# Kernel tuning notes

Measured on AMD Instinct MI355X. Metric: run time of the kernel, lower is better.

## Reference

```python
import jax, jax.numpy as jnp
import numpy as np

WS, SHIFT, NH, DIM = 8, 4, 4, 128
HD = DIM // NH
B, H, W = 16, 128, 128
N = WS * WS
LOG100 = float(np.log(100.0))


def _rel_tables():
    r = np.arange(-(WS - 1), WS, dtype=np.float32)
    tab = np.stack(np.meshgrid(r, r, indexing='ij'), axis=-1) / (WS - 1) * 8.0
    tab = np.sign(tab) * np.log2(np.abs(tab) + 1.0) / np.log2(8.0)
    coords = np.stack(np.meshgrid(np.arange(WS), np.arange(WS), indexing='ij')).reshape(2, -1)
    rel = (coords[:, :, None] - coords[:, None, :]).transpose(1, 2, 0).copy()
    rel[:, :, 0] += WS - 1
    rel[:, :, 1] += WS - 1
    rel[:, :, 0] *= 2 * WS - 1
    return jnp.asarray(tab.reshape(-1, 2)), jnp.asarray(rel.sum(-1))

REL_TABLE, REL_INDEX = _rel_tables()  # ((2WS-1)^2, 2), (N, N)


def _attn_mask():
    img = np.zeros((H, W), np.float32)
    cnt = 0
    for hs in (slice(0, -WS), slice(-WS, -SHIFT), slice(-SHIFT, None)):
        for ws in (slice(0, -WS), slice(-WS, -SHIFT), slice(-SHIFT, None)):
            img[hs, ws] = cnt
            cnt += 1
    mw = img.reshape(H // WS, WS, W // WS, WS).transpose(0, 2, 1, 3).reshape(-1, N)
    d = mw[:, None, :] - mw[:, :, None]
    return jnp.asarray(np.where(d != 0, -100.0, 0.0).astype(np.float32))

ATTN_MASK = _attn_mask()  # (nW, N, N)


def _ln(x, w, b, eps=1e-5):
    mu = x.mean(-1, keepdims=True)
    var = ((x - mu) ** 2).mean(-1, keepdims=True)
    return (x - mu) * jax.lax.rsqrt(var + eps) * w + b


def setup_inputs() -> dict:
    key = jax.random.key(0)
    ks = jax.random.split(key, 8)
    s = 0.02
    return {
        'x': jax.random.normal(ks[0], (B, DIM, H, W), jnp.float32),
        'norm1_w': jnp.ones((DIM,), jnp.float32),
        'norm1_b': jnp.zeros((DIM,), jnp.float32),
        'qkv_w': jax.random.normal(ks[1], (3 * DIM, DIM), jnp.float32) * s,
        'q_bias': jnp.zeros((DIM,), jnp.float32),
        'v_bias': jnp.zeros((DIM,), jnp.float32),
        'logit_scale': jnp.full((NH, 1, 1), float(np.log(10.0)), jnp.float32),
        'cpb_w1': jax.random.normal(ks[2], (512, 2), jnp.float32) * s,
        'cpb_b1': jnp.zeros((512,), jnp.float32),
        'cpb_w2': jax.random.normal(ks[3], (NH, 512), jnp.float32) * s,
        'proj_w': jax.random.normal(ks[4], (DIM, DIM), jnp.float32) * s,
        'proj_b': jnp.zeros((DIM,), jnp.float32),
        'norm2_w': jnp.ones((DIM,), jnp.float32),
        'norm2_b': jnp.zeros((DIM,), jnp.float32),
        'fc1_w': jax.random.normal(ks[5], (4 * DIM, DIM), jnp.float32) * s,
        'fc1_b': jnp.zeros((4 * DIM,), jnp.float32),
        'fc2_w': jax.random.normal(ks[6], (DIM, 4 * DIM), jnp.float32) * s,
        'fc2_b': jnp.zeros((DIM,), jnp.float32),
    }


def reference(x, norm1_w, norm1_b, qkv_w, q_bias, v_bias, logit_scale,
              cpb_w1, cpb_b1, cpb_w2, proj_w, proj_b,
              norm2_w, norm2_b, fc1_w, fc1_b, fc2_w, fc2_b):
    xb = jnp.transpose(x, (0, 2, 3, 1))                 # (B,H,W,C)
    shortcut = xb.reshape(B, H * W, DIM)
    shifted = jnp.roll(xb, (-SHIFT, -SHIFT), axis=(1, 2))
    # window partition -> (B*nW, N, C)
    xw = shifted.reshape(B, H // WS, WS, W // WS, WS, DIM)
    xw = xw.transpose(0, 1, 3, 2, 4, 5).reshape(-1, N, DIM)
    B_ = xw.shape[0]
    qkv_bias = jnp.concatenate([q_bias, jnp.zeros_like(v_bias), v_bias])
    qkv = xw @ qkv_w.T + qkv_bias
    qkv = qkv.reshape(B_, N, 3, NH, HD).transpose(2, 0, 3, 1, 4)
    q, k, v = qkv[0], qkv[1], qkv[2]                    # (B_,NH,N,HD)
    qn = q / jnp.maximum(jnp.linalg.norm(q, axis=-1, keepdims=True), 1e-12)
    kn = k / jnp.maximum(jnp.linalg.norm(k, axis=-1, keepdims=True), 1e-12)
    attn = jnp.einsum('bhnd,bhmd->bhnm', qn, kn)
    attn = attn * jnp.exp(jnp.minimum(logit_scale, LOG100))
    # continuous relative position bias: tiny MLP over log-spaced coords + gather
    tab = jax.nn.relu(REL_TABLE @ cpb_w1.T + cpb_b1) @ cpb_w2.T    # ((2WS-1)^2, NH)
    bias = tab[REL_INDEX.reshape(-1)].reshape(N, N, NH).transpose(2, 0, 1)
    attn = attn + (16.0 * jax.nn.sigmoid(bias))[None]
    nW = ATTN_MASK.shape[0]
    attn = attn.reshape(B_ // nW, nW, NH, N, N) + ATTN_MASK[None, :, None]
    attn = jax.nn.softmax(attn.reshape(B_, NH, N, N), axis=-1)
    out = jnp.einsum('bhnm,bhmd->bhnd', attn, v).transpose(0, 2, 1, 3).reshape(B_, N, DIM)
    out = out @ proj_w.T + proj_b
    # window reverse + reverse cyclic shift
    out = out.reshape(B, H // WS, W // WS, WS, WS, DIM).transpose(0, 1, 3, 2, 4, 5).reshape(B, H, W, DIM)
    out = jnp.roll(out, (SHIFT, SHIFT), axis=(1, 2)).reshape(B, H * W, DIM)
    x1 = shortcut + _ln(out, norm1_w, norm1_b)          # Swin-v2 post-norm residual
    hdn = jax.nn.silu(x1 @ fc1_w.T + fc1_b) @ fc2_w.T + fc2_b
    x2 = x1 + _ln(hdn, norm2_w, norm2_b)
    return x2.reshape(B, H, W, DIM).transpose(0, 3, 1, 2)
```

## Files before the change

kernel.cpp:

```cpp
#include <hip/hip_runtime.h>
#include <cstdint>
#include <cstddef>

typedef __bf16 bf16;
typedef __bf16 bf16x8 __attribute__((ext_vector_type(8)));
typedef float f32x4 __attribute__((ext_vector_type(4)));

#define MFMA16(a, b, c) __builtin_amdgcn_mfma_f32_16x16x32_bf16((a), (b), (c), 0, 0, 0)

__device__ __forceinline__ float bf2f(bf16 v) { return (float)v; }

#define OFF_SCALES 65536
#define OFF_FLAG   65552
#define OFF_QKVB   65600
#define OFF_PROJB  67136
#define OFF_N1W    67648
#define OFF_N1B    68160
#define OFF_FC1B   68672
#define OFF_FC2B   70720
#define OFF_N2W    71232
#define OFF_N2B    71744
#define OFF_QKVW   73728
#define OFF_PROJW  172032
#define OFF_FC1W   204800
#define OFF_FC2W   335872

template<int DT>
__device__ __forceinline__ void g_ld4(const void* base, size_t idx, float* o) {
    if constexpr (DT == 0) {
        uint2 d = *(const uint2*)((const bf16*)base + idx);
        const bf16* p = (const bf16*)&d;
        o[0] = bf2f(p[0]); o[1] = bf2f(p[1]); o[2] = bf2f(p[2]); o[3] = bf2f(p[3]);
    } else {
        float4 d = *(const float4*)((const float*)base + idx);
        o[0] = d.x; o[1] = d.y; o[2] = d.z; o[3] = d.w;
    }
}

__global__ void k_precompute(const void* __restrict__ cpb_w1, const void* __restrict__ cpb_b1,
                             const void* __restrict__ cpb_w2, const void* __restrict__ logit_scale,
                             const void* __restrict__ qkv_w_raw,
                             float* __restrict__ biasAll, float* __restrict__ scales,
                             int* __restrict__ flag)
{
    __shared__ float w1s[1024];
    __shared__ float b1s[512];
    __shared__ float w2s[2048];
    __shared__ float tabv[225][4];
    __shared__ int s_cnt;
    const int t = threadIdx.x;
    if (t == 0) s_cnt = 0;
    __syncthreads();
    {
        const unsigned short* u = (const unsigned short*)qkv_w_raw;
        int c = 0;
        for (int i = t; i < 1024; i += 256) {
            const int e = (u[i] >> 7) & 0xFF;
            if (e >= 0x90 || (e != 0 && e <= 0x60)) ++c;
        }
        atomicAdd(&s_cnt, c);
    }
    __syncthreads();
    const int isf = (s_cnt > 64) ? 1 : 0;
    if (t == 0) *flag = isf;
    if (isf) {
        const float* w1 = (const float*)cpb_w1;
        const float* b1 = (const float*)cpb_b1;
        const float* w2 = (const float*)cpb_w2;
        for (int i = t; i < 1024; i += 256) w1s[i] = w1[i];
        for (int i = t; i < 512;  i += 256) b1s[i] = b1[i];
        for (int i = t; i < 2048; i += 256) w2s[i] = w2[i];
        if (t < 4) scales[t] = expf(fminf(((const float*)logit_scale)[t], 4.6051701859880914f));
    } else {
        const bf16* w1 = (const bf16*)cpb_w1;
        const bf16* b1 = (const bf16*)cpb_b1;
        const bf16* w2 = (const bf16*)cpb_w2;
        for (int i = t; i < 1024; i += 256) w1s[i] = bf2f(w1[i]);
        for (int i = t; i < 512;  i += 256) b1s[i] = bf2f(b1[i]);
        for (int i = t; i < 2048; i += 256) w2s[i] = bf2f(w2[i]);
        if (t < 4) scales[t] = expf(fminf(bf2f(((const bf16*)logit_scale)[t]), 4.6051701859880914f));
    }
    __syncthreads();
    if (t < 225) {
        const int i = t / 15, j = t % 15;
        auto relf = [](int tt) -> float {
            float tf = (float)tt * (8.0f / 7.0f);
            float a = log2f(fabsf(tf) + 1.0f) * (1.0f / 3.0f);
            return tt < 0 ? -a : a;
        };
        const float x0 = relf(i - 7), x1 = relf(j - 7);
        float a0 = 0.f, a1 = 0.f, a2 = 0.f, a3 = 0.f;
        for (int jj = 0; jj < 512; ++jj) {
            float hv = w1s[jj*2] * x0 + w1s[jj*2+1] * x1 + b1s[jj];
            hv = fmaxf(hv, 0.0f);
            a0 += w2s[jj]        * hv;
            a1 += w2s[512 + jj]  * hv;
            a2 += w2s[1024 + jj] * hv;
            a3 += w2s[1536 + jj] * hv;
        }
        tabv[t][0] = a0; tabv[t][1] = a1; tabv[t][2] = a2; tabv[t][3] = a3;
    }
    __syncthreads();
    for (int idx = t; idx < 4*64*64; idx += 256) {
        const int h = idx >> 12, rem = idx & 4095, i = rem >> 6, j = rem & 63;
        const int di = (i >> 3) - (j >> 3) + 7;
        const int dj = (i & 7) - (j & 7) + 7;
        const float bv = tabv[di*15 + dj][h];
        biasAll[idx] = 16.0f / (1.0f + expf(-bv));
    }
}

__global__ void k_convert(
    const void* __restrict__ qkv_w, const void* __restrict__ proj_w,
    const void* __restrict__ fc1w, const void* __restrict__ fc2w,
    const void* __restrict__ q_bias, const void* __restrict__ v_bias,
    const void* __restrict__ proj_b, const void* __restrict__ n1w, const void* __restrict__ n1b,
    const void* __restrict__ fc1b, const void* __restrict__ fc2b,
    const void* __restrict__ n2w, const void* __restrict__ n2b,
    const int* __restrict__ flag, char* __restrict__ ws)
{
    const int isf = *flag;
    const int g  = blockIdx.x * 256 + threadIdx.x;
    const int gs = gridDim.x * 256;
    bf16* qw = (bf16*)(ws + OFF_QKVW);
    bf16* pw = (bf16*)(ws + OFF_PROJW);
    bf16* f1 = (bf16*)(ws + OFF_FC1W);
    bf16* f2 = (bf16*)(ws + OFF_FC2W);
    if (isf) {
        const float* a = (const float*)qkv_w;  for (int i = g; i < 49152; i += gs) qw[i] = (bf16)a[i];
        const float* b = (const float*)proj_w; for (int i = g; i < 16384; i += gs) pw[i] = (bf16)b[i];
        const float* c = (const float*)fc1w;   for (int i = g; i < 65536; i += gs) f1[i] = (bf16)c[i];
        const float* d = (const float*)fc2w;   for (int i = g; i < 65536; i += gs) f2[i] = (bf16)d[i];
    } else {
        const bf16* a = (const bf16*)qkv_w;  for (int i = g; i < 49152; i += gs) qw[i] = a[i];
        const bf16* b = (const bf16*)proj_w; for (int i = g; i < 16384; i += gs) pw[i] = b[i];
        const bf16* c = (const bf16*)fc1w;   for (int i = g; i < 65536; i += gs) f1[i] = c[i];
        const bf16* d = (const bf16*)fc2w;   for (int i = g; i < 65536; i += gs) f2[i] = d[i];
    }
    auto ldf = [&](const void* p, int i) -> float {
        return isf ? ((const float*)p)[i] : bf2f(((const bf16*)p)[i]);
    };
    float* qb  = (float*)(ws + OFF_QKVB);
    float* pb  = (float*)(ws + OFF_PROJB);
    float* w1  = (float*)(ws + OFF_N1W);
    float* b1  = (float*)(ws + OFF_N1B);
    float* f1b = (float*)(ws + OFF_FC1B);
    float* f2b = (float*)(ws + OFF_FC2B);
    float* w2  = (float*)(ws + OFF_N2W);
    float* b2  = (float*)(ws + OFF_N2B);
    for (int i = g; i < 384; i += gs)
        qb[i] = (i < 128) ? ldf(q_bias, i) : ((i < 256) ? 0.0f : ldf(v_bias, i - 256));
    for (int i = g; i < 512; i += gs) f1b[i] = ldf(fc1b, i);
    for (int i = g; i < 128; i += gs) {
        pb[i]  = ldf(proj_b, i); w1[i] = ldf(n1w, i); b1[i] = ldf(n1b, i);
        f2b[i] = ldf(fc2b, i);   w2[i] = ldf(n2w, i); b2[i] = ldf(n2b, i);
    }
}

template<int DT>
__global__ __launch_bounds__(256, 2) void k_fused(
    const void* __restrict__ x,
    const bf16* __restrict__ qkvw, const float* __restrict__ qkvb,
    const bf16* __restrict__ projw, const float* __restrict__ projb,
    const float* __restrict__ n1wf, const float* __restrict__ n1bf,
    const bf16* __restrict__ fc1w, const float* __restrict__ fc1bf,
    const bf16* __restrict__ fc2w, const float* __restrict__ fc2bf,
    const float* __restrict__ n2wf, const float* __restrict__ n2bf,
    const float* __restrict__ biasAll, const float* __restrict__ scales,
    const int* __restrict__ flag, void* __restrict__ out)
{
    if (*flag != DT) return;

    __shared__ __align__(16) char smem[75008];
    bf16* Xs    = (bf16*)smem;
    bf16* qkvs  = (bf16*)(smem + 17408);
    bf16* Ps    = qkvs;
    bf16* x1s   = qkvs;
    bf16* vs    = (bf16*)(smem + 54272);
    bf16* Os    = vs;
    bf16* hs    = vs;
    float* invqs = (float*)(smem + 72704);
    float* invks = (float*)(smem + 73728);
    int*   rid   = (int*)(smem + 74752);
    float* psum = invqs;
    float* pvar = invks;

    const int tid  = threadIdx.x;
    const int wv   = tid >> 6;
    const int lane = tid & 63;
    const int l15  = lane & 15;
    const int quad = lane >> 4;

    const int bid0 = blockIdx.x;
    const int bid  = ((bid0 & 7) << 9) | (bid0 >> 3);
    const int b   = bid >> 8;
    const int wh  = (bid >> 4) & 15;
    const int ww  = bid & 15;

    {
        const int c  = tid & 127;
        const int rb = tid >> 7;
        const int w0 = ww*8 + 4;
        const int w1 = (ww*8 + 8) & 127;
#pragma unroll
        for (int k = 0; k < 4; ++k) {
            const int r    = k*2 + rb;
            const int srch = (wh*8 + r + 4) & 127;
            const size_t rowbase = (((size_t)(b*128 + c))*128 + srch)*128;
            float va[4], vb[4];
            g_ld4<DT>(x, rowbase + w0, va);
            g_ld4<DT>(x, rowbase + w1, vb);
#pragma unroll
            for (int j = 0; j < 4; ++j) {
                Xs[(r*8 + j)*136 + c]     = (bf16)va[j];
                Xs[(r*8 + 4 + j)*136 + c] = (bf16)vb[j];
            }
        }
        if (tid < 64) {
            const int rr = tid >> 3, cc = tid & 7;
            const int hs_ = wh*8 + rr, wsc = ww*8 + cc;
            const int rh = (hs_ < 120) ? 0 : ((hs_ < 124) ? 1 : 2);
            const int rw = (wsc < 120) ? 0 : ((wsc < 124) ? 1 : 2);
            rid[tid] = rh*3 + rw;
        }
    }
    __syncthreads();

    {
        f32x4 acc[4][6];
#pragma unroll
        for (int mt = 0; mt < 4; ++mt)
#pragma unroll
            for (int nl = 0; nl < 6; ++nl) acc[mt][nl] = (f32x4){0.f, 0.f, 0.f, 0.f};
#pragma unroll
        for (int ks = 0; ks < 4; ++ks) {
            bf16x8 a[4];
#pragma unroll
            for (int mt = 0; mt < 4; ++mt)
                a[mt] = *(const bf16x8*)&Xs[(mt*16 + l15)*136 + ks*32 + quad*8];
#pragma unroll
            for (int nl = 0; nl < 6; ++nl) {
                const int o = (wv*6 + nl)*16 + l15;
                bf16x8 bw = *(const bf16x8*)&qkvw[(size_t)o*128 + ks*32 + quad*8];
#pragma unroll
                for (int mt = 0; mt < 4; ++mt)
                    acc[mt][nl] = MFMA16(a[mt], bw, acc[mt][nl]);
            }
        }
#pragma unroll
        for (int nl = 0; nl < 6; ++nl) {
            const int col = (wv*6 + nl)*16 + l15;
            const float bias = qkvb[col];
#pragma unroll
            for (int mt = 0; mt < 4; ++mt)
#pragma unroll
                for (int r = 0; r < 4; ++r) {
                    const int row = mt*16 + quad*4 + r;
                    const float v = acc[mt][nl][r] + bias;
                    if (col < 256) qkvs[row*264 + col] = (bf16)v;
                    else           vs[(col - 256)*72 + row] = (bf16)v;
                }
        }
    }
    __syncthreads();

    {
        const int n = lane;
        const bf16* qrow = &qkvs[n*264 + wv*32];
        const bf16* krow = &qkvs[n*264 + 128 + wv*32];
        float sq = 0.f, sk = 0.f;
#pragma unroll
        for (int dd = 0; dd < 4; ++dd) {
            bf16x8 vq = *(const bf16x8*)(qrow + dd*8);
            bf16x8 vk = *(const bf16x8*)(krow + dd*8);
#pragma unroll
            for (int e = 0; e < 8; ++e) {
                const float fq = (float)vq[e]; sq += fq*fq;
                const float fk = (float)vk[e]; sk += fk*fk;
            }
        }
        invqs[wv*64 + n] = 1.0f / fmaxf(sqrtf(sq), 1e-12f);
        invks[wv*64 + n] = 1.0f / fmaxf(sqrtf(sk), 1e-12f);
    }
    __syncthreads();

    {
        const float scale = scales[wv];
        f32x4 s[4][4];
#pragma unroll
        for (int mt = 0; mt < 4; ++mt)
#pragma unroll
            for (int nt = 0; nt < 4; ++nt) s[mt][nt] = (f32x4){0.f, 0.f, 0.f, 0.f};
        bf16x8 aq[4];
#pragma unroll
        for (int mt = 0; mt < 4; ++mt)
            aq[mt] = *(const bf16x8*)&qkvs[(mt*16 + l15)*264 + wv*32 + quad*8];
#pragma unroll
        for (int nt = 0; nt < 4; ++nt) {
            bf16x8 bk = *(const bf16x8*)&qkvs[(nt*16 + l15)*264 + 128 + wv*32 + quad*8];
#pragma unroll
            for (int mt = 0; mt < 4; ++mt)
                s[mt][nt] = MFMA16(aq[mt], bk, s[mt][nt]);
        }
        __syncthreads();
        const float* bg = biasAll + wv*4096;
        const bool bnd = (wh == 15) || (ww == 15);
        float ikj[4]; int rj[4];
#pragma unroll
        for (int nt = 0; nt < 4; ++nt) {
            ikj[nt] = invks[wv*64 + nt*16 + l15];
            rj[nt]  = rid[nt*16 + l15];
        }
#pragma unroll
        for (int mt = 0; mt < 4; ++mt)
#pragma unroll
            for (int r = 0; r < 4; ++r) {
                const int i = mt*16 + quad*4 + r;
                const float iqs = invqs[wv*64 + i] * scale;
                const int ri = rid[i];
#pragma unroll
                for (int nt = 0; nt < 4; ++nt) {
                    const int j = nt*16 + l15;
                    float v = s[mt][nt][r] * (iqs * ikj[nt]) + bg[i*64 + j];
                    if (bnd && (ri != rj[nt])) v -= 100.0f;
                    s[mt][nt][r] = v;
                }
            }
#pragma unroll
        for (int mt = 0; mt < 4; ++mt) {
            float mx[4], sm[4];
#pragma unroll
            for (int r = 0; r < 4; ++r) {
                float m = fmaxf(fmaxf(s[mt][0][r], s[mt][1][r]), fmaxf(s[mt][2][r], s[mt][3][r]));
                m = fmaxf(m, __shfl_xor(m, 1));
                m = fmaxf(m, __shfl_xor(m, 2));
                m = fmaxf(m, __shfl_xor(m, 4));
                m = fmaxf(m, __shfl_xor(m, 8));
                mx[r] = m; sm[r] = 0.f;
            }
#pragma unroll
            for (int nt = 0; nt < 4; ++nt)
#pragma unroll
                for (int r = 0; r < 4; ++r) {
                    const float e = __expf(s[mt][nt][r] - mx[r]);
                    s[mt][nt][r] = e;
                    sm[r] += e;
                }
#pragma unroll
            for (int r = 0; r < 4; ++r) {
                float t2 = sm[r];
                t2 += __shfl_xor(t2, 1);
                t2 += __shfl_xor(t2, 2);
                t2 += __shfl_xor(t2, 4);
                t2 += __shfl_xor(t2, 8);
                sm[r] = 1.0f / t2;
            }
#pragma unroll
            for (int nt = 0; nt < 4; ++nt)
#pragma unroll
                for (int r = 0; r < 4; ++r) {
                    const float p = s[mt][nt][r] * sm[r];
                    Ps[wv*64*72 + (mt*16 + quad*4 + r)*72 + nt*16 + l15] = (bf16)p;
                }
        }
    }
    __syncthreads();

    {
        f32x4 o[4][2];
#pragma unroll
        for (int mt = 0; mt < 4; ++mt)
#pragma unroll
            for (int nt = 0; nt < 2; ++nt) o[mt][nt] = (f32x4){0.f, 0.f, 0.f, 0.f};
#pragma unroll
        for (int ks = 0; ks < 2; ++ks) {
            bf16x8 ap[4];
#pragma unroll
            for (int mt = 0; mt < 4; ++mt)
                ap[mt] = *(const bf16x8*)&Ps[wv*64*72 + (mt*16 + l15)*72 + ks*32 + quad*8];
#pragma unroll
            for (int nt = 0; nt < 2; ++nt) {
                bf16x8 bv = *(const bf16x8*)&vs[(wv*32 + nt*16 + l15)*72 + ks*32 + quad*8];
#pragma unroll
                for (int mt = 0; mt < 4; ++mt)
                    o[mt][nt] = MFMA16(ap[mt], bv, o[mt][nt]);
            }
        }
        __syncthreads();
#pragma unroll
        for (int mt = 0; mt < 4; ++mt)
#pragma unroll
            for (int nt = 0; nt < 2; ++nt)
#pragma unroll
                for (int r = 0; r < 4; ++r) {
                    const int i = mt*16 + quad*4 + r;
                    Os[i*136 + wv*32 + nt*16 + l15] = (bf16)o[mt][nt][r];
                }
    }
    __syncthreads();

    {
        f32x4 pa[4][2];
#pragma unroll
        for (int mt = 0; mt < 4; ++mt)
#pragma unroll
            for (int nt = 0; nt < 2; ++nt) pa[mt][nt] = (f32x4){0.f, 0.f, 0.f, 0.f};
#pragma unroll
        for (int ks = 0; ks < 4; ++ks) {
            bf16x8 ao[4];
#pragma unroll
            for (int mt = 0; mt < 4; ++mt)
                ao[mt] = *(const bf16x8*)&Os[(mt*16 + l15)*136 + ks*32 + quad*8];
#pragma unroll
            for (int nt = 0; nt < 2; ++nt) {
                const int oc = wv*32 + nt*16 + l15;
                bf16x8 bw = *(const bf16x8*)&projw[(size_t)oc*128 + ks*32 + quad*8];
#pragma unroll
                for (int mt = 0; mt < 4; ++mt)
                    pa[mt][nt] = MFMA16(ao[mt], bw, pa[mt][nt]);
            }
        }
        float pb[2], wn[2], bn[2];
#pragma unroll
        for (int nt = 0; nt < 2; ++nt) {
            const int oc = wv*32 + nt*16 + l15;
            pb[nt] = projb[oc]; wn[nt] = n1wf[oc]; bn[nt] = n1bf[oc];
        }
#pragma unroll
        for (int mt = 0; mt < 4; ++mt)
#pragma unroll
            for (int r = 0; r < 4; ++r) {
                pa[mt][0][r] += pb[0];
                pa[mt][1][r] += pb[1];
                float sv = pa[mt][0][r] + pa[mt][1][r];
                sv += __shfl_xor(sv, 1); sv += __shfl_xor(sv, 2);
                sv += __shfl_xor(sv, 4); sv += __shfl_xor(sv, 8);
                if (l15 == 0) psum[wv*64 + mt*16 + quad*4 + r] = sv;
            }
        __syncthreads();
        float mu[4][4];
#pragma unroll
        for (int mt = 0; mt < 4; ++mt)
#pragma unroll
            for (int r = 0; r < 4; ++r) {
                const int i = mt*16 + quad*4 + r;
                mu[mt][r] = (psum[i] + psum[64+i] + psum[128+i] + psum[192+i]) * (1.0f/128.0f);
                const float d0 = pa[mt][0][r] - mu[mt][r];
                const float d1 = pa[mt][1][r] - mu[mt][r];
                float sv = d0*d0 + d1*d1;
                sv += __shfl_xor(sv, 1); sv += __shfl_xor(sv, 2);
                sv += __shfl_xor(sv, 4); sv += __shfl_xor(sv, 8);
                if (l15 == 0) pvar[wv*64 + i] = sv;
            }
        __syncthreads();
#pragma unroll
        for (int mt = 0; mt < 4; ++mt)
#pragma unroll
            for (int r = 0; r < 4; ++r) {
                const int i = mt*16 + quad*4 + r;
                const float var = (pvar[i] + pvar[64+i] + pvar[128+i] + pvar[192+i]) * (1.0f/128.0f);
                const float rstd = rsqrtf(var + 1e-5f);
#pragma unroll
                for (int nt = 0; nt < 2; ++nt) {
                    const int oc = wv*32 + nt*16 + l15;
                    const float y = (pa[mt][nt][r] - mu[mt][r]) * rstd * wn[nt] + bn[nt];
                    const float x1v = bf2f(Xs[i*136 + oc]) + y;
                    x1s[i*136 + oc] = (bf16)x1v;
                }
            }
    }
    __syncthreads();

    f32x4 ya[4][2];
#pragma unroll
    for (int mt = 0; mt < 4; ++mt)
#pragma unroll
        for (int nt = 0; nt < 2; ++nt) ya[mt][nt] = (f32x4){0.f, 0.f, 0.f, 0.f};

#pragma unroll
    for (int ch = 0; ch < 4; ++ch) {
        if (ch) __syncthreads();
        f32x4 ha[4][2];
#pragma unroll
        for (int mt = 0; mt < 4; ++mt)
#pragma unroll
            for (int nt = 0; nt < 2; ++nt) ha[mt][nt] = (f32x4){0.f, 0.f, 0.f, 0.f};
#pragma unroll
        for (int ks = 0; ks < 4; ++ks) {
            bf16x8 a[4];
#pragma unroll
            for (int mt = 0; mt < 4; ++mt)
                a[mt] = *(const bf16x8*)&x1s[(mt*16 + l15)*136 + ks*32 + quad*8];
#pragma unroll
            for (int nt = 0; nt < 2; ++nt) {
                const int hid = ch*128 + wv*32 + nt*16 + l15;
                bf16x8 bw = *(const bf16x8*)&fc1w[(size_t)hid*128 + ks*32 + quad*8];
#pragma unroll
                for (int mt = 0; mt < 4; ++mt)
                    ha[mt][nt] = MFMA16(a[mt], bw, ha[mt][nt]);
            }
        }
#pragma unroll
        for (int nt = 0; nt < 2; ++nt) {
            const int hid = ch*128 + wv*32 + nt*16 + l15;
            const float bb = fc1bf[hid];
            const int hl = wv*32 + nt*16 + l15;
#pragma unroll
            for (int mt = 0; mt < 4; ++mt)
#pragma unroll
                for (int r = 0; r < 4; ++r) {
                    float v = ha[mt][nt][r] + bb;
                    v = v / (1.0f + __expf(-v));
                    hs[(mt*16 + quad*4 + r)*136 + hl] = (bf16)v;
                }
        }
        __syncthreads();
#pragma unroll
        for (int ks = 0; ks < 4; ++ks) {
            bf16x8 ah[4];
#pragma unroll
            for (int mt = 0; mt < 4; ++mt)
                ah[mt] = *(const bf16x8*)&hs[(mt*16 + l15)*136 + ks*32 + quad*8];
#pragma unroll
            for (int nt = 0; nt < 2; ++nt) {
                const int oc = wv*32 + nt*16 + l15;
                bf16x8 bw = *(const bf16x8*)&fc2w[(size_t)oc*512 + ch*128 + ks*32 + quad*8];
#pragma unroll
                for (int mt = 0; mt < 4; ++mt)
                    ya[mt][nt] = MFMA16(ah[mt], bw, ya[mt][nt]);
            }
        }
    }
    __syncthreads();

    {
        float pb[2], wn[2], bn[2];
#pragma unroll
        for (int nt = 0; nt < 2; ++nt) {
            const int oc = wv*32 + nt*16 + l15;
            pb[nt] = fc2bf[oc]; wn[nt] = n2wf[oc]; bn[nt] = n2bf[oc];
        }
#pragma unroll
        for (int mt = 0; mt < 4; ++mt)
#pragma unroll
            for (int r = 0; r < 4; ++r) {
                ya[mt][0][r] += pb[0];
                ya[mt][1][r] += pb[1];
                float sv = ya[mt][0][r] + ya[mt][1][r];
                sv += __shfl_xor(sv, 1); sv += __shfl_xor(sv, 2);
                sv += __shfl_xor(sv, 4); sv += __shfl_xor(sv, 8);
                if (l15 == 0) psum[wv*64 + mt*16 + quad*4 + r] = sv;
            }
        __syncthreads();
        float mu[4][4];
#pragma unroll
        for (int mt = 0; mt < 4; ++mt)
#pragma unroll
            for (int r = 0; r < 4; ++r) {
                const int i = mt*16 + quad*4 + r;
                mu[mt][r] = (psum[i] + psum[64+i] + psum[128+i] + psum[192+i]) * (1.0f/128.0f);
                const float d0 = ya[mt][0][r] - mu[mt][r];
                const float d1 = ya[mt][1][r] - mu[mt][r];
                float sv = d0*d0 + d1*d1;
                sv += __shfl_xor(sv, 1); sv += __shfl_xor(sv, 2);
                sv += __shfl_xor(sv, 4); sv += __shfl_xor(sv, 8);
                if (l15 == 0) pvar[wv*64 + i] = sv;
            }
        __syncthreads();
        bf16* x2s = hs;
#pragma unroll
        for (int mt = 0; mt < 4; ++mt)
#pragma unroll
            for (int r = 0; r < 4; ++r) {
                const int i = mt*16 + quad*4 + r;
                const float var = (pvar[i] + pvar[64+i] + pvar[128+i] + pvar[192+i]) * (1.0f/128.0f);
                const float rstd = rsqrtf(var + 1e-5f);
#pragma unroll
                for (int nt = 0; nt < 2; ++nt) {
                    const int oc = wv*32 + nt*16 + l15;
                    const float yv = (ya[mt][nt][r] - mu[mt][r]) * rstd * wn[nt] + bn[nt];
                    const float x2v = bf2f(x1s[i*136 + oc]) + yv;
                    x2s[i*136 + oc] = (bf16)x2v;
                }
            }
    }
    __syncthreads();

    {
        const bf16* x2s = hs;
        const int wf0 = ww*8 + 4;
        const int wf1 = (ww*8 + 8) & 127;
#pragma unroll
        for (int g = 0; g < 4; ++g) {
            const int idx = g*256 + tid;
            const int c  = idx & 127;
            const int rr = idx >> 7;
            const int hf = (wh*8 + rr + 4) & 127;
            const size_t rowb = ((size_t)(b*128 + c))*16384 + (size_t)hf*128;
            if constexpr (DT == 0) {
                const unsigned short* xu = (const unsigned short*)x2s;
                uint2 u0, u1;
                u0.x = (unsigned)xu[(rr*8+0)*136 + c] | ((unsigned)xu[(rr*8+1)*136 + c] << 16);
                u0.y = (unsigned)xu[(rr*8+2)*136 + c] | ((unsigned)xu[(rr*8+3)*136 + c] << 16);
                u1.x = (unsigned)xu[(rr*8+4)*136 + c] | ((unsigned)xu[(rr*8+5)*136 + c] << 16);
                u1.y = (unsigned)xu[(rr*8+6)*136 + c] | ((unsigned)xu[(rr*8+7)*136 + c] << 16);
                bf16* dstb = (bf16*)out;
                *(uint2*)(dstb + rowb + wf0) = u0;
                *(uint2*)(dstb + rowb + wf1) = u1;
            } else {
                float4 u0, u1;
                u0.x = bf2f(x2s[(rr*8+0)*136 + c]); u0.y = bf2f(x2s[(rr*8+1)*136 + c]);
                u0.z = bf2f(x2s[(rr*8+2)*136 + c]); u0.w = bf2f(x2s[(rr*8+3)*136 + c]);
                u1.x = bf2f(x2s[(rr*8+4)*136 + c]); u1.y = bf2f(x2s[(rr*8+5)*136 + c]);
                u1.z = bf2f(x2s[(rr*8+6)*136 + c]); u1.w = bf2f(x2s[(rr*8+7)*136 + c]);
                float* dstf = (float*)out;
                *(float4*)(dstf + rowb + wf0) = u0;
                *(float4*)(dstf + rowb + wf1) = u1;
            }
        }
    }
}

extern "C" void kernel_launch(void* const* d_in, const int* in_sizes, int n_in,
                              void* d_out, int out_size, void* d_ws, size_t ws_size,
                              hipStream_t stream)
{
    (void)in_sizes; (void)n_in; (void)out_size; (void)ws_size;
    const void* x      = d_in[0];
    const void* n1w    = d_in[1];
    const void* n1b    = d_in[2];
    const void* qkv_w  = d_in[3];
    const void* q_bias = d_in[4];
    const void* v_bias = d_in[5];
    const void* lscale = d_in[6];
    const void* cpb_w1 = d_in[7];
    const void* cpb_b1 = d_in[8];
    const void* cpb_w2 = d_in[9];
    const void* proj_w = d_in[10];
    const void* proj_b = d_in[11];
    const void* n2w    = d_in[12];
    const void* n2b    = d_in[13];
    const void* fc1w   = d_in[14];
    const void* fc1b   = d_in[15];
    const void* fc2w   = d_in[16];
    const void* fc2b   = d_in[17];

    char*  ws      = (char*)d_ws;
    float* biasAll = (float*)ws;
    float* scales  = (float*)(ws + OFF_SCALES);
    int*   flag    = (int*)(ws + OFF_FLAG);

    k_precompute<<<dim3(1), dim3(256), 0, stream>>>(cpb_w1, cpb_b1, cpb_w2, lscale, qkv_w,
                                                    biasAll, scales, flag);
    k_convert<<<dim3(96), dim3(256), 0, stream>>>(qkv_w, proj_w, fc1w, fc2w,
                                                  q_bias, v_bias, proj_b, n1w, n1b,
                                                  fc1b, fc2b, n2w, n2b, flag, ws);
    k_fused<0><<<dim3(4096), dim3(256), 0, stream>>>(x,
        (const bf16*)(ws + OFF_QKVW), (const float*)(ws + OFF_QKVB),
        (const bf16*)(ws + OFF_PROJW), (const float*)(ws + OFF_PROJB),
        (const float*)(ws + OFF_N1W), (const float*)(ws + OFF_N1B),
        (const bf16*)(ws + OFF_FC1W), (const float*)(ws + OFF_FC1B),
        (const bf16*)(ws + OFF_FC2W), (const float*)(ws + OFF_FC2B),
        (const float*)(ws + OFF_N2W), (const float*)(ws + OFF_N2B),
        biasAll, scales, flag, d_out);
    k_fused<1><<<dim3(4096), dim3(256), 0, stream>>>(x,
        (const bf16*)(ws + OFF_QKVW), (const float*)(ws + OFF_QKVB),
        (const bf16*)(ws + OFF_PROJW), (const float*)(ws + OFF_PROJB),
        (const float*)(ws + OFF_N1W), (const float*)(ws + OFF_N1B),
        (const bf16*)(ws + OFF_FC1W), (const float*)(ws + OFF_FC1B),
        (const bf16*)(ws + OFF_FC2W), (const float*)(ws + OFF_FC2B),
        (const float*)(ws + OFF_N2W), (const float*)(ws + OFF_N2B),
        biasAll, scales, flag, d_out);
}
```

Measured before the change: 701.4 us.

## Transpose MFMA operand roles for packed stores, merge init kernels, single fused launch

Swaps MFMA A/B operand order in the QKV, attention, and MLP stages so each lane's accumulator holds four consecutive output channels. This lets results be written to shared memory as packed 4-element bf16 stores, and LayerNorm reductions use cross-quad shuffles instead of 16-lane ones. The precompute and convert kernels are merged into one launch. The two dtype-templated fused launches become one kernel that branches on the runtime flag. This removes two launches and scalar LDS stores, at the cost of runtime dtype branches inside the fused kernel.

```diff
diff --git a/kernel.cpp b/kernel.cpp
--- a/kernel.cpp
+++ b/kernel.cpp
@@ -3,12 +3,18 @@
 #include <cstddef>
 
 typedef __bf16 bf16;
+typedef __bf16 bf16x4 __attribute__((ext_vector_type(4)));
 typedef __bf16 bf16x8 __attribute__((ext_vector_type(8)));
 typedef float f32x4 __attribute__((ext_vector_type(4)));
 
 #define MFMA16(a, b, c) __builtin_amdgcn_mfma_f32_16x16x32_bf16((a), (b), (c), 0, 0, 0)
 
 __device__ __forceinline__ float bf2f(bf16 v) { return (float)v; }
+
+__device__ __forceinline__ void pack4(float a0, float a1, float a2, float a3, bf16* dst) {
+    bf16x4 v; v[0] = (bf16)a0; v[1] = (bf16)a1; v[2] = (bf16)a2; v[3] = (bf16)a3;
+    *(bf16x4*)dst = v;
+}
 
 #define OFF_SCALES 65536
 #define OFF_FLAG   65552
@@ -37,22 +43,22 @@
     }
 }
 
-__global__ void k_precompute(const void* __restrict__ cpb_w1, const void* __restrict__ cpb_b1,
-                             const void* __restrict__ cpb_w2, const void* __restrict__ logit_scale,
-                             const void* __restrict__ qkv_w_raw,
-                             float* __restrict__ biasAll, float* __restrict__ scales,
-                             int* __restrict__ flag)
+__global__ void k_init(const void* __restrict__ cpb_w1, const void* __restrict__ cpb_b1,
+                       const void* __restrict__ cpb_w2, const void* __restrict__ logit_scale,
+                       const void* __restrict__ qkv_w, const void* __restrict__ proj_w,
+                       const void* __restrict__ fc1w, const void* __restrict__ fc2w,
+                       const void* __restrict__ q_bias, const void* __restrict__ v_bias,
+                       const void* __restrict__ proj_b, const void* __restrict__ n1w, const void* __restrict__ n1b,
+                       const void* __restrict__ fc1b, const void* __restrict__ fc2b,
+                       const void* __restrict__ n2w, const void* __restrict__ n2b,
+                       char* __restrict__ ws)
 {
-    __shared__ float w1s[1024];
-    __shared__ float b1s[512];
-    __shared__ float w2s[2048];
-    __shared__ float tabv[225][4];
+    const int t = threadIdx.x;
     __shared__ int s_cnt;
-    const int t = threadIdx.x;
     if (t == 0) s_cnt = 0;
     __syncthreads();
     {
-        const unsigned short* u = (const unsigned short*)qkv_w_raw;
+        const unsigned short* u = (const unsigned short*)qkv_w;
         int c = 0;
         for (int i = t; i < 1024; i += 256) {
             const int e = (u[i] >> 7) & 0xFF;
@@ -62,102 +68,100 @@
     }
     __syncthreads();
     const int isf = (s_cnt > 64) ? 1 : 0;
-    if (t == 0) *flag = isf;
-    if (isf) {
-        const float* w1 = (const float*)cpb_w1;
-        const float* b1 = (const float*)cpb_b1;
-        const float* w2 = (const float*)cpb_w2;
-        for (int i = t; i < 1024; i += 256) w1s[i] = w1[i];
-        for (int i = t; i < 512;  i += 256) b1s[i] = b1[i];
-        for (int i = t; i < 2048; i += 256) w2s[i] = w2[i];
-        if (t < 4) scales[t] = expf(fminf(((const float*)logit_scale)[t], 4.6051701859880914f));
+
+    if (blockIdx.x == 0) {
+        float* biasAll = (float*)ws;
+        float* scales  = (float*)(ws + OFF_SCALES);
+        int*   flag    = (int*)(ws + OFF_FLAG);
+        if (t == 0) *flag = isf;
+        __shared__ float w1s[1024];
+        __shared__ float b1s[512];
+        __shared__ float w2s[2048];
+        __shared__ float tabv[225][4];
+        if (isf) {
+            const float* w1 = (const float*)cpb_w1;
+            const float* b1 = (const float*)cpb_b1;
+            const float* w2 = (const float*)cpb_w2;
+            for (int i = t; i < 1024; i += 256) w1s[i] = w1[i];
+            for (int i = t; i < 512;  i += 256) b1s[i] = b1[i];
+            for (int i = t; i < 2048; i += 256) w2s[i] = w2[i];
+            if (t < 4) scales[t] = expf(fminf(((const float*)logit_scale)[t], 4.6051701859880914f));
+        } else {
+            const bf16* w1 = (const bf16*)cpb_w1;
+            const bf16* b1 = (const bf16*)cpb_b1;
+            const bf16* w2 = (const bf16*)cpb_w2;
+            for (int i = t; i < 1024; i += 256) w1s[i] = bf2f(w1[i]);
+            for (int i = t; i < 512;  i += 256) b1s[i] = bf2f(b1[i]);
+            for (int i = t; i < 2048; i += 256) w2s[i] = bf2f(w2[i]);
+            if (t < 4) scales[t] = expf(fminf(bf2f(((const bf16*)logit_scale)[t]), 4.6051701859880914f));
+        }
+        __syncthreads();
+        if (t < 225) {
+            const int i = t / 15, j = t % 15;
+            auto relf = [](int tt) -> float {
+                float tf = (float)tt * (8.0f / 7.0f);
+                float a = log2f(fabsf(tf) + 1.0f) * (1.0f / 3.0f);
+                return tt < 0 ? -a : a;
+            };
+            const float x0 = relf(i - 7), x1 = relf(j - 7);
+            float a0 = 0.f, a1 = 0.f, a2 = 0.f, a3 = 0.f;
+            for (int jj = 0; jj < 512; ++jj) {
+                float hv = w1s[jj*2] * x0 + w1s[jj*2+1] * x1 + b1s[jj];
+                hv = fmaxf(hv, 0.0f);
+                a0 += w2s[jj]        * hv;
+                a1 += w2s[512 + jj]  * hv;
+                a2 += w2s[1024 + jj] * hv;
+                a3 += w2s[1536 + jj] * hv;
+            }
+            tabv[t][0] = a0; tabv[t][1] = a1; tabv[t][2] = a2; tabv[t][3] = a3;
+        }
+        __syncthreads();
+        for (int idx = t; idx < 4*64*64; idx += 256) {
+            const int h = idx >> 12, rem = idx & 4095, i = rem >> 6, j = rem & 63;
+            const int di = (i >> 3) - (j >> 3) + 7;
+            const int dj = (i & 7) - (j & 7) + 7;
+            const float bv = tabv[di*15 + dj][h];
+            biasAll[idx] = 16.0f / (1.0f + expf(-bv));
+        }
     } else {
-        const bf16* w1 = (const bf16*)cpb_w1;
-        const bf16* b1 = (const bf16*)cpb_b1;
-        const bf16* w2 = (const bf16*)cpb_w2;
-        for (int i = t; i < 1024; i += 256) w1s[i] = bf2f(w1[i]);
-        for (int i = t; i < 512;  i += 256) b1s[i] = bf2f(b1[i]);
-        for (int i = t; i < 2048; i += 256) w2s[i] = bf2f(w2[i]);
-        if (t < 4) scales[t] = expf(fminf(bf2f(((const bf16*)logit_scale)[t]), 4.6051701859880914f));
-    }
-    __syncthreads();
-    if (t < 225) {
-        const int i = t / 15, j = t % 15;
-        auto relf = [](int tt) -> float {
-            float tf = (float)tt * (8.0f / 7.0f);
-            float a = log2f(fabsf(tf) + 1.0f) * (1.0f / 3.0f);
-            return tt < 0 ? -a : a;
+        const int g  = (blockIdx.x - 1) * 256 + t;
+        const int gs = 96 * 256;
+        bf16* qw = (bf16*)(ws + OFF_QKVW);
+        bf16* pw = (bf16*)(ws + OFF_PROJW);
+        bf16* f1 = (bf16*)(ws + OFF_FC1W);
+        bf16* f2 = (bf16*)(ws + OFF_FC2W);
+        if (isf) {
+            const float* a = (const float*)qkv_w;  for (int i = g; i < 49152; i += gs) qw[i] = (bf16)a[i];
+            const float* b = (const float*)proj_w; for (int i = g; i < 16384; i += gs) pw[i] = (bf16)b[i];
+            const float* c = (const float*)fc1w;   for (int i = g; i < 65536; i += gs) f1[i] = (bf16)c[i];
+            const float* d = (const float*)fc2w;   for (int i = g; i < 65536; i += gs) f2[i] = (bf16)d[i];
+        } else {
+            const bf16* a = (const bf16*)qkv_w;  for (int i = g; i < 49152; i += gs) qw[i] = a[i];
+            const bf16* b = (const bf16*)proj_w; for (int i = g; i < 16384; i += gs) pw[i] = b[i];
+            const bf16* c = (const bf16*)fc1w;   for (int i = g; i < 65536; i += gs) f1[i] = c[i];
+            const bf16* d = (const bf16*)fc2w;   for (int i = g; i < 65536; i += gs) f2[i] = d[i];
+        }
+        auto ldf = [&](const void* p, int i) -> float {
+            return isf ? ((const float*)p)[i] : bf2f(((const bf16*)p)[i]);
         };
-        const float x0 = relf(i - 7), x1 = relf(j - 7);
-        float a0 = 0.f, a1 = 0.f, a2 = 0.f, a3 = 0.f;
-        for (int jj = 0; jj < 512; ++jj) {
-            float hv = w1s[jj*2] * x0 + w1s[jj*2+1] * x1 + b1s[jj];
-            hv = fmaxf(hv, 0.0f);
-            a0 += w2s[jj]        * hv;
-            a1 += w2s[512 + jj]  * hv;
-            a2 += w2s[1024 + jj] * hv;
-            a3 += w2s[1536 + jj] * hv;
-        }
-        tabv[t][0] = a0; tabv[t][1] = a1; tabv[t][2] = a2; tabv[t][3] = a3;
-    }
-    __syncthreads();
-    for (int idx = t; idx < 4*64*64; idx += 256) {
-        const int h = idx >> 12, rem = idx & 4095, i = rem >> 6, j = rem & 63;
-        const int di = (i >> 3) - (j >> 3) + 7;
-        const int dj = (i & 7) - (j & 7) + 7;
-        const float bv = tabv[di*15 + dj][h];
-        biasAll[idx] = 16.0f / (1.0f + expf(-bv));
+        float* qb  = (float*)(ws + OFF_QKVB);
+        float* pb  = (float*)(ws + OFF_PROJB);
+        float* w1  = (float*)(ws + OFF_N1W);
+        float* b1  = (float*)(ws + OFF_N1B);
+        float* f1b = (float*)(ws + OFF_FC1B);
+        float* f2b = (float*)(ws + OFF_FC2B);
+        float* w2  = (float*)(ws + OFF_N2W);
+        float* b2  = (float*)(ws + OFF_N2B);
+        for (int i = g; i < 384; i += gs)
+            qb[i] = (i < 128) ? ldf(q_bias, i) : ((i < 256) ? 0.0f : ldf(v_bias, i - 256));
+        for (int i = g; i < 512; i += gs) f1b[i] = ldf(fc1b, i);
+        for (int i = g; i < 128; i += gs) {
+            pb[i]  = ldf(proj_b, i); w1[i] = ldf(n1w, i); b1[i] = ldf(n1b, i);
+            f2b[i] = ldf(fc2b, i);   w2[i] = ldf(n2w, i); b2[i] = ldf(n2b, i);
+        }
     }
 }
 
-__global__ void k_convert(
-    const void* __restrict__ qkv_w, const void* __restrict__ proj_w,
-    const void* __restrict__ fc1w, const void* __restrict__ fc2w,
-    const void* __restrict__ q_bias, const void* __restrict__ v_bias,
-    const void* __restrict__ proj_b, const void* __restrict__ n1w, const void* __restrict__ n1b,
-    const void* __restrict__ fc1b, const void* __restrict__ fc2b,
-    const void* __restrict__ n2w, const void* __restrict__ n2b,
-    const int* __restrict__ flag, char* __restrict__ ws)
-{
-    const int isf = *flag;
-    const int g  = blockIdx.x * 256 + threadIdx.x;
-    const int gs = gridDim.x * 256;
-    bf16* qw = (bf16*)(ws + OFF_QKVW);
-    bf16* pw = (bf16*)(ws + OFF_PROJW);
-    bf16* f1 = (bf16*)(ws + OFF_FC1W);
-    bf16* f2 = (bf16*)(ws + OFF_FC2W);
-    if (isf) {
-        const float* a = (const float*)qkv_w;  for (int i = g; i < 49152; i += gs) qw[i] = (bf16)a[i];
-        const float* b = (const float*)proj_w; for (int i = g; i < 16384; i += gs) pw[i] = (bf16)b[i];
-        const float* c = (const float*)fc1w;   for (int i = g; i < 65536; i += gs) f1[i] = (bf16)c[i];
-        const float* d = (const float*)fc2w;   for (int i = g; i < 65536; i += gs) f2[i] = (bf16)d[i];
-    } else {
-        const bf16* a = (const bf16*)qkv_w;  for (int i = g; i < 49152; i += gs) qw[i] = a[i];
-        const bf16* b = (const bf16*)proj_w; for (int i = g; i < 16384; i += gs) pw[i] = b[i];
-        const bf16* c = (const bf16*)fc1w;   for (int i = g; i < 65536; i += gs) f1[i] = c[i];
-        const bf16* d = (const bf16*)fc2w;   for (int i = g; i < 65536; i += gs) f2[i] = d[i];
-    }
-    auto ldf = [&](const void* p, int i) -> float {
-        return isf ? ((const float*)p)[i] : bf2f(((const bf16*)p)[i]);
-    };
-    float* qb  = (float*)(ws + OFF_QKVB);
-    float* pb  = (float*)(ws + OFF_PROJB);
-    float* w1  = (float*)(ws + OFF_N1W);
-    float* b1  = (float*)(ws + OFF_N1B);
-    float* f1b = (float*)(ws + OFF_FC1B);
-    float* f2b = (float*)(ws + OFF_FC2B);
-    float* w2  = (float*)(ws + OFF_N2W);
-    float* b2  = (float*)(ws + OFF_N2B);
-    for (int i = g; i < 384; i += gs)
-        qb[i] = (i < 128) ? ldf(q_bias, i) : ((i < 256) ? 0.0f : ldf(v_bias, i - 256));
-    for (int i = g; i < 512; i += gs) f1b[i] = ldf(fc1b, i);
-    for (int i = g; i < 128; i += gs) {
-        pb[i]  = ldf(proj_b, i); w1[i] = ldf(n1w, i); b1[i] = ldf(n1b, i);
-        f2b[i] = ldf(fc2b, i);   w2[i] = ldf(n2w, i); b2[i] = ldf(n2b, i);
-    }
-}
-
-template<int DT>
 __global__ __launch_bounds__(256, 2) void k_fused(
     const void* __restrict__ x,
     const bf16* __restrict__ qkvw, const float* __restrict__ qkvb,
@@ -169,12 +173,12 @@
     const float* __restrict__ biasAll, const float* __restrict__ scales,
     const int* __restrict__ flag, void* __restrict__ out)
 {
-    if (*flag != DT) return;
+    const int isf = *flag;
 
     __shared__ __align__(16) char smem[75008];
     bf16* Xs    = (bf16*)smem;
     bf16* qkvs  = (bf16*)(smem + 17408);
-    bf16* Ps    = qkvs;
+    bf16* PsT   = qkvs;
     bf16* x1s   = qkvs;
     bf16* vs    = (bf16*)(smem + 54272);
     bf16* Os    = vs;
@@ -208,8 +212,8 @@
             const int srch = (wh*8 + r + 4) & 127;
             const size_t rowbase = (((size_t)(b*128 + c))*128 + srch)*128;
             float va[4], vb[4];
-            g_ld4<DT>(x, rowbase + w0, va);
-            g_ld4<DT>(x, rowbase + w1, vb);
+            if (isf) { g_ld4<1>(x, rowbase + w0, va); g_ld4<1>(x, rowbase + w1, vb); }
+            else     { g_ld4<0>(x, rowbase + w0, va); g_ld4<0>(x, rowbase + w1, vb); }
 #pragma unroll
             for (int j = 0; j < 4; ++j) {
                 Xs[(r*8 + j)*136 + c]     = (bf16)va[j];
@@ -227,11 +231,11 @@
     __syncthreads();
 
     {
-        f32x4 acc[4][6];
-#pragma unroll
-        for (int mt = 0; mt < 4; ++mt)
-#pragma unroll
-            for (int nl = 0; nl < 6; ++nl) acc[mt][nl] = (f32x4){0.f, 0.f, 0.f, 0.f};
+        f32x4 acc[6][4];
+#pragma unroll
+        for (int nl = 0; nl < 6; ++nl)
+#pragma unroll
+            for (int mt = 0; mt < 4; ++mt) acc[nl][mt] = (f32x4){0.f, 0.f, 0.f, 0.f};
 #pragma unroll
         for (int ks = 0; ks < 4; ++ks) {
             bf16x8 a[4];
@@ -240,26 +244,38 @@
                 a[mt] = *(const bf16x8*)&Xs[(mt*16 + l15)*136 + ks*32 + quad*8];
 #pragma unroll
             for (int nl = 0; nl < 6; ++nl) {
-                const int o = (wv*6 + nl)*16 + l15;
-                bf16x8 bw = *(const bf16x8*)&qkvw[(size_t)o*128 + ks*32 + quad*8];
+                const int tile = wv*6 + nl;
+                bf16x8 bw = *(const bf16x8*)&qkvw[(size_t)(tile*16 + l15)*128 + ks*32 + quad*8];
+                if (tile < 16) {
+#pragma unroll
+                    for (int mt = 0; mt < 4; ++mt)
+                        acc[nl][mt] = MFMA16(bw, a[mt], acc[nl][mt]);
+                } else {
+#pragma unroll
+                    for (int mt = 0; mt < 4; ++mt)
+                        acc[nl][mt] = MFMA16(a[mt], bw, acc[nl][mt]);
+                }
+            }
+        }
+#pragma unroll
+        for (int nl = 0; nl < 6; ++nl) {
+            const int tile = wv*6 + nl;
+            const int ctb  = tile*16;
+            if (ctb < 256) {
+                const float4 qb4 = *(const float4*)&qkvb[ctb + quad*4];
 #pragma unroll
                 for (int mt = 0; mt < 4; ++mt)
-                    acc[mt][nl] = MFMA16(a[mt], bw, acc[mt][nl]);
-            }
-        }
-#pragma unroll
-        for (int nl = 0; nl < 6; ++nl) {
-            const int col = (wv*6 + nl)*16 + l15;
-            const float bias = qkvb[col];
-#pragma unroll
-            for (int mt = 0; mt < 4; ++mt)
-#pragma unroll
-                for (int r = 0; r < 4; ++r) {
-                    const int row = mt*16 + quad*4 + r;
-                    const float v = acc[mt][nl][r] + bias;
-                    if (col < 256) qkvs[row*264 + col] = (bf16)v;
-                    else           vs[(col - 256)*72 + row] = (bf16)v;
-                }
+                    pack4(acc[nl][mt][0] + qb4.x, acc[nl][mt][1] + qb4.y,
+                          acc[nl][mt][2] + qb4.z, acc[nl][mt][3] + qb4.w,
+                          &qkvs[(mt*16 + l15)*264 + ctb + quad*4]);
+            } else {
+                const float bb = qkvb[ctb + l15];
+#pragma unroll
+                for (int mt = 0; mt < 4; ++mt)
+                    pack4(acc[nl][mt][0] + bb, acc[nl][mt][1] + bb,
+                          acc[nl][mt][2] + bb, acc[nl][mt][3] + bb,
+                          &vs[(ctb - 256 + l15)*72 + mt*16 + quad*4]);
+            }
         }
     }
     __syncthreads();
@@ -288,301 +304,308 @@
         const float scale = scales[wv];
         f32x4 s[4][4];
 #pragma unroll
-        for (int mt = 0; mt < 4; ++mt)
-#pragma unroll
-            for (int nt = 0; nt < 4; ++nt) s[mt][nt] = (f32x4){0.f, 0.f, 0.f, 0.f};
+        for (int jt = 0; jt < 4; ++jt)
+#pragma unroll
+            for (int it = 0; it < 4; ++it) s[jt][it] = (f32x4){0.f, 0.f, 0.f, 0.f};
         bf16x8 aq[4];
 #pragma unroll
-        for (int mt = 0; mt < 4; ++mt)
-            aq[mt] = *(const bf16x8*)&qkvs[(mt*16 + l15)*264 + wv*32 + quad*8];
-#pragma unroll
-        for (int nt = 0; nt < 4; ++nt) {
-            bf16x8 bk = *(const bf16x8*)&qkvs[(nt*16 + l15)*264 + 128 + wv*32 + quad*8];
-#pragma unroll
-            for (int mt = 0; mt < 4; ++mt)
-                s[mt][nt] = MFMA16(aq[mt], bk, s[mt][nt]);
-        }
-        __syncthreads();
+        for (int it = 0; it < 4; ++it)
+            aq[it] = *(const bf16x8*)&qkvs[(it*16 + l15)*264 + wv*32 + quad*8];
+#pragma unroll
+        for (int jt = 0; jt < 4; ++jt) {
+            bf16x8 bk = *(const bf16x8*)&qkvs[(jt*16 + l15)*264 + 128 + wv*32 + quad*8];
+#pragma unroll
+            for (int it = 0; it < 4; ++it)
+                s[jt][it] = MFMA16(bk, aq[it], s[jt][it]);
+        }
+        __syncthreads();
+
         const float* bg = biasAll + wv*4096;
         const bool bnd = (wh == 15) || (ww == 15);
-        float ikj[4]; int rj[4];
-#pragma unroll
-        for (int nt = 0; nt < 4; ++nt) {
-            ikj[nt] = invks[wv*64 + nt*16 + l15];
-            rj[nt]  = rid[nt*16 + l15];
-        }
-#pragma unroll
-        for (int mt = 0; mt < 4; ++mt)
-#pragma unroll
-            for (int r = 0; r < 4; ++r) {
-                const int i = mt*16 + quad*4 + r;
-                const float iqs = invqs[wv*64 + i] * scale;
-                const int ri = rid[i];
-#pragma unroll
-                for (int nt = 0; nt < 4; ++nt) {
-                    const int j = nt*16 + l15;
-                    float v = s[mt][nt][r] * (iqs * ikj[nt]) + bg[i*64 + j];
-                    if (bnd && (ri != rj[nt])) v -= 100.0f;
-                    s[mt][nt][r] = v;
-                }
-            }
-#pragma unroll
-        for (int mt = 0; mt < 4; ++mt) {
-            float mx[4], sm[4];
-#pragma unroll
-            for (int r = 0; r < 4; ++r) {
-                float m = fmaxf(fmaxf(s[mt][0][r], s[mt][1][r]), fmaxf(s[mt][2][r], s[mt][3][r]));
-                m = fmaxf(m, __shfl_xor(m, 1));
-                m = fmaxf(m, __shfl_xor(m, 2));
-                m = fmaxf(m, __shfl_xor(m, 4));
-                m = fmaxf(m, __shfl_xor(m, 8));
-                mx[r] = m; sm[r] = 0.f;
-            }
-#pragma unroll
-            for (int nt = 0; nt < 4; ++nt)
+        float iqs[4]; int ri[4];
+#pragma unroll
+        for (int it = 0; it < 4; ++it) {
+            iqs[it] = invqs[wv*64 + it*16 + l15] * scale;
+            ri[it]  = rid[it*16 + l15];
+        }
+        float4 ikj[4]; int4 rj4[4];
+#pragma unroll
+        for (int jt = 0; jt < 4; ++jt) {
+            ikj[jt] = *(const float4*)&invks[wv*64 + jt*16 + quad*4];
+            rj4[jt] = *(const int4*)&rid[jt*16 + quad*4];
+        }
+#pragma unroll
+        for (int it = 0; it < 4; ++it) {
+            const int i = it*16 + l15;
+#pragma unroll
+            for (int jt = 0; jt < 4; ++jt) {
+                const float4 bb = *(const float4*)&bg[i*64 + jt*16 + quad*4];
 #pragma unroll
                 for (int r = 0; r < 4; ++r) {
-                    const float e = __expf(s[mt][nt][r] - mx[r]);
-                    s[mt][nt][r] = e;
-                    sm[r] += e;
-                }
-#pragma unroll
-            for (int r = 0; r < 4; ++r) {
-                float t2 = sm[r];
-                t2 += __shfl_xor(t2, 1);
-                t2 += __shfl_xor(t2, 2);
-                t2 += __shfl_xor(t2, 4);
-                t2 += __shfl_xor(t2, 8);
-                sm[r] = 1.0f / t2;
-            }
-#pragma unroll
-            for (int nt = 0; nt < 4; ++nt)
+                    float v = s[jt][it][r] * (iqs[it] * ((const float*)&ikj[jt])[r]) + ((const float*)&bb)[r];
+                    if (bnd && (ri[it] != ((const int*)&rj4[jt])[r])) v -= 100.0f;
+                    s[jt][it][r] = v;
+                }
+            }
+            float m = s[0][it][0];
+#pragma unroll
+            for (int jt = 0; jt < 4; ++jt)
+#pragma unroll
+                for (int r = 0; r < 4; ++r) m = fmaxf(m, s[jt][it][r]);
+            m = fmaxf(m, __shfl_xor(m, 16));
+            m = fmaxf(m, __shfl_xor(m, 32));
+            float sm = 0.f;
+#pragma unroll
+            for (int jt = 0; jt < 4; ++jt)
 #pragma unroll
                 for (int r = 0; r < 4; ++r) {
-                    const float p = s[mt][nt][r] * sm[r];
-                    Ps[wv*64*72 + (mt*16 + quad*4 + r)*72 + nt*16 + l15] = (bf16)p;
-                }
-        }
-    }
-    __syncthreads();
-
-    {
-        f32x4 o[4][2];
-#pragma unroll
-        for (int mt = 0; mt < 4; ++mt)
-#pragma unroll
-            for (int nt = 0; nt < 2; ++nt) o[mt][nt] = (f32x4){0.f, 0.f, 0.f, 0.f};
+                    const float e = __expf(s[jt][it][r] - m);
+                    s[jt][it][r] = e;
+                    sm += e;
+                }
+            sm += __shfl_xor(sm, 16);
+            sm += __shfl_xor(sm, 32);
+            const float inv = 1.0f / sm;
+#pragma unroll
+            for (int jt = 0; jt < 4; ++jt)
+                pack4(s[jt][it][0]*inv, s[jt][it][1]*inv, s[jt][it][2]*inv, s[jt][it][3]*inv,
+                      &PsT[wv*4608 + i*72 + jt*16 + quad*4]);
+        }
+    }
+    __syncthreads();
+
+    {
+        f32x4 o[2][4];
+#pragma unroll
+        for (int dt = 0; dt < 2; ++dt)
+#pragma unroll
+            for (int it = 0; it < 4; ++it) o[dt][it] = (f32x4){0.f, 0.f, 0.f, 0.f};
 #pragma unroll
         for (int ks = 0; ks < 2; ++ks) {
-            bf16x8 ap[4];
-#pragma unroll
-            for (int mt = 0; mt < 4; ++mt)
-                ap[mt] = *(const bf16x8*)&Ps[wv*64*72 + (mt*16 + l15)*72 + ks*32 + quad*8];
-#pragma unroll
-            for (int nt = 0; nt < 2; ++nt) {
-                bf16x8 bv = *(const bf16x8*)&vs[(wv*32 + nt*16 + l15)*72 + ks*32 + quad*8];
-#pragma unroll
-                for (int mt = 0; mt < 4; ++mt)
-                    o[mt][nt] = MFMA16(ap[mt], bv, o[mt][nt]);
-            }
-        }
-        __syncthreads();
-#pragma unroll
-        for (int mt = 0; mt < 4; ++mt)
-#pragma unroll
-            for (int nt = 0; nt < 2; ++nt)
+            bf16x8 bp[4];
+#pragma unroll
+            for (int it = 0; it < 4; ++it)
+                bp[it] = *(const bf16x8*)&PsT[wv*4608 + (it*16 + l15)*72 + ks*32 + quad*8];
+#pragma unroll
+            for (int dt = 0; dt < 2; ++dt) {
+                bf16x8 av = *(const bf16x8*)&vs[(wv*32 + dt*16 + l15)*72 + ks*32 + quad*8];
+#pragma unroll
+                for (int it = 0; it < 4; ++it)
+                    o[dt][it] = MFMA16(av, bp[it], o[dt][it]);
+            }
+        }
+        __syncthreads();
+#pragma unroll
+        for (int dt = 0; dt < 2; ++dt)
+#pragma unroll
+            for (int it = 0; it < 4; ++it)
+                pack4(o[dt][it][0], o[dt][it][1], o[dt][it][2], o[dt][it][3],
+                      &Os[(it*16 + l15)*136 + wv*32 + dt*16 + quad*4]);
+    }
+    __syncthreads();
+
+    {
+        f32x4 pa[2][4];
+#pragma unroll
+        for (int ct = 0; ct < 2; ++ct)
+#pragma unroll
+            for (int tt = 0; tt < 4; ++tt) pa[ct][tt] = (f32x4){0.f, 0.f, 0.f, 0.f};
+#pragma unroll
+        for (int ks = 0; ks < 4; ++ks) {
+            bf16x8 bo[4];
+#pragma unroll
+            for (int tt = 0; tt < 4; ++tt)
+                bo[tt] = *(const bf16x8*)&Os[(tt*16 + l15)*136 + ks*32 + quad*8];
+#pragma unroll
+            for (int ct = 0; ct < 2; ++ct) {
+                bf16x8 aw = *(const bf16x8*)&projw[(size_t)(wv*32 + ct*16 + l15)*128 + ks*32 + quad*8];
+#pragma unroll
+                for (int tt = 0; tt < 4; ++tt)
+                    pa[ct][tt] = MFMA16(aw, bo[tt], pa[ct][tt]);
+            }
+        }
+        float4 pb4[2], wn4[2], bn4[2];
+#pragma unroll
+        for (int ct = 0; ct < 2; ++ct) {
+            const int ob = wv*32 + ct*16 + quad*4;
+            pb4[ct] = *(const float4*)&projb[ob];
+            wn4[ct] = *(const float4*)&n1wf[ob];
+            bn4[ct] = *(const float4*)&n1bf[ob];
+        }
+#pragma unroll
+        for (int tt = 0; tt < 4; ++tt) {
+            float sv = 0.f;
+#pragma unroll
+            for (int ct = 0; ct < 2; ++ct)
 #pragma unroll
                 for (int r = 0; r < 4; ++r) {
-                    const int i = mt*16 + quad*4 + r;
-                    Os[i*136 + wv*32 + nt*16 + l15] = (bf16)o[mt][nt][r];
-                }
-    }
-    __syncthreads();
-
-    {
-        f32x4 pa[4][2];
-#pragma unroll
-        for (int mt = 0; mt < 4; ++mt)
-#pragma unroll
-            for (int nt = 0; nt < 2; ++nt) pa[mt][nt] = (f32x4){0.f, 0.f, 0.f, 0.f};
-#pragma unroll
-        for (int ks = 0; ks < 4; ++ks) {
-            bf16x8 ao[4];
-#pragma unroll
-            for (int mt = 0; mt < 4; ++mt)
-                ao[mt] = *(const bf16x8*)&Os[(mt*16 + l15)*136 + ks*32 + quad*8];
-#pragma unroll
-            for (int nt = 0; nt < 2; ++nt) {
-                const int oc = wv*32 + nt*16 + l15;
-                bf16x8 bw = *(const bf16x8*)&projw[(size_t)oc*128 + ks*32 + quad*8];
-#pragma unroll
-                for (int mt = 0; mt < 4; ++mt)
-                    pa[mt][nt] = MFMA16(ao[mt], bw, pa[mt][nt]);
-            }
-        }
-        float pb[2], wn[2], bn[2];
-#pragma unroll
-        for (int nt = 0; nt < 2; ++nt) {
-            const int oc = wv*32 + nt*16 + l15;
-            pb[nt] = projb[oc]; wn[nt] = n1wf[oc]; bn[nt] = n1bf[oc];
-        }
-#pragma unroll
-        for (int mt = 0; mt < 4; ++mt)
-#pragma unroll
-            for (int r = 0; r < 4; ++r) {
-                pa[mt][0][r] += pb[0];
-                pa[mt][1][r] += pb[1];
-                float sv = pa[mt][0][r] + pa[mt][1][r];
-                sv += __shfl_xor(sv, 1); sv += __shfl_xor(sv, 2);
-                sv += __shfl_xor(sv, 4); sv += __shfl_xor(sv, 8);
-                if (l15 == 0) psum[wv*64 + mt*16 + quad*4 + r] = sv;
-            }
-        __syncthreads();
-        float mu[4][4];
-#pragma unroll
-        for (int mt = 0; mt < 4; ++mt)
-#pragma unroll
-            for (int r = 0; r < 4; ++r) {
-                const int i = mt*16 + quad*4 + r;
-                mu[mt][r] = (psum[i] + psum[64+i] + psum[128+i] + psum[192+i]) * (1.0f/128.0f);
-                const float d0 = pa[mt][0][r] - mu[mt][r];
-                const float d1 = pa[mt][1][r] - mu[mt][r];
-                float sv = d0*d0 + d1*d1;
-                sv += __shfl_xor(sv, 1); sv += __shfl_xor(sv, 2);
-                sv += __shfl_xor(sv, 4); sv += __shfl_xor(sv, 8);
-                if (l15 == 0) pvar[wv*64 + i] = sv;
-            }
-        __syncthreads();
-#pragma unroll
-        for (int mt = 0; mt < 4; ++mt)
-#pragma unroll
-            for (int r = 0; r < 4; ++r) {
-                const int i = mt*16 + quad*4 + r;
-                const float var = (pvar[i] + pvar[64+i] + pvar[128+i] + pvar[192+i]) * (1.0f/128.0f);
-                const float rstd = rsqrtf(var + 1e-5f);
-#pragma unroll
-                for (int nt = 0; nt < 2; ++nt) {
-                    const int oc = wv*32 + nt*16 + l15;
-                    const float y = (pa[mt][nt][r] - mu[mt][r]) * rstd * wn[nt] + bn[nt];
-                    const float x1v = bf2f(Xs[i*136 + oc]) + y;
-                    x1s[i*136 + oc] = (bf16)x1v;
-                }
-            }
-    }
-    __syncthreads();
-
-    f32x4 ya[4][2];
-#pragma unroll
-    for (int mt = 0; mt < 4; ++mt)
-#pragma unroll
-        for (int nt = 0; nt < 2; ++nt) ya[mt][nt] = (f32x4){0.f, 0.f, 0.f, 0.f};
+                    pa[ct][tt][r] += ((const float*)&pb4[ct])[r];
+                    sv += pa[ct][tt][r];
+                }
+            sv += __shfl_xor(sv, 16);
+            sv += __shfl_xor(sv, 32);
+            if (quad == 0) psum[wv*64 + tt*16 + l15] = sv;
+        }
+        __syncthreads();
+        float mu[4];
+#pragma unroll
+        for (int tt = 0; tt < 4; ++tt) {
+            const int tok = tt*16 + l15;
+            mu[tt] = (psum[tok] + psum[64+tok] + psum[128+tok] + psum[192+tok]) * (1.0f/128.0f);
+            float sv = 0.f;
+#pragma unroll
+            for (int ct = 0; ct < 2; ++ct)
+#pragma unroll
+                for (int r = 0; r < 4; ++r) {
+                    const float d = pa[ct][tt][r] - mu[tt];
+                    sv += d*d;
+                }
+            sv += __shfl_xor(sv, 16);
+            sv += __shfl_xor(sv, 32);
+            if (quad == 0) pvar[wv*64 + tok] = sv;
+        }
+        __syncthreads();
+#pragma unroll
+        for (int tt = 0; tt < 4; ++tt) {
+            const int tok = tt*16 + l15;
+            const float var = (pvar[tok] + pvar[64+tok] + pvar[128+tok] + pvar[192+tok]) * (1.0f/128.0f);
+            const float rstd = rsqrtf(var + 1e-5f);
+#pragma unroll
+            for (int ct = 0; ct < 2; ++ct) {
+                const int ob = wv*32 + ct*16 + quad*4;
+                bf16x4 xr = *(const bf16x4*)&Xs[tok*136 + ob];
+                float xv[4];
+#pragma unroll
+                for (int r = 0; r < 4; ++r)
+                    xv[r] = bf2f(xr[r]) + (pa[ct][tt][r] - mu[tt]) * rstd * ((const float*)&wn4[ct])[r]
+                            + ((const float*)&bn4[ct])[r];
+                pack4(xv[0], xv[1], xv[2], xv[3], &x1s[tok*136 + ob]);
+            }
+        }
+    }
+    __syncthreads();
+
+    f32x4 ya[2][4];
+#pragma unroll
+    for (int ct = 0; ct < 2; ++ct)
+#pragma unroll
+        for (int tt = 0; tt < 4; ++tt) ya[ct][tt] = (f32x4){0.f, 0.f, 0.f, 0.f};
 
 #pragma unroll
     for (int ch = 0; ch < 4; ++ch) {
         if (ch) __syncthreads();
-        f32x4 ha[4][2];
-#pragma unroll
-        for (int mt = 0; mt < 4; ++mt)
-#pragma unroll
-            for (int nt = 0; nt < 2; ++nt) ha[mt][nt] = (f32x4){0.f, 0.f, 0.f, 0.f};
+        f32x4 ha[2][4];
+#pragma unroll
+        for (int ht = 0; ht < 2; ++ht)
+#pragma unroll
+            for (int tt = 0; tt < 4; ++tt) ha[ht][tt] = (f32x4){0.f, 0.f, 0.f, 0.f};
 #pragma unroll
         for (int ks = 0; ks < 4; ++ks) {
-            bf16x8 a[4];
-#pragma unroll
-            for (int mt = 0; mt < 4; ++mt)
-                a[mt] = *(const bf16x8*)&x1s[(mt*16 + l15)*136 + ks*32 + quad*8];
-#pragma unroll
-            for (int nt = 0; nt < 2; ++nt) {
-                const int hid = ch*128 + wv*32 + nt*16 + l15;
-                bf16x8 bw = *(const bf16x8*)&fc1w[(size_t)hid*128 + ks*32 + quad*8];
-#pragma unroll
-                for (int mt = 0; mt < 4; ++mt)
-                    ha[mt][nt] = MFMA16(a[mt], bw, ha[mt][nt]);
-            }
-        }
-#pragma unroll
-        for (int nt = 0; nt < 2; ++nt) {
-            const int hid = ch*128 + wv*32 + nt*16 + l15;
-            const float bb = fc1bf[hid];
-            const int hl = wv*32 + nt*16 + l15;
-#pragma unroll
-            for (int mt = 0; mt < 4; ++mt)
+            bf16x8 bx[4];
+#pragma unroll
+            for (int tt = 0; tt < 4; ++tt)
+                bx[tt] = *(const bf16x8*)&x1s[(tt*16 + l15)*136 + ks*32 + quad*8];
+#pragma unroll
+            for (int ht = 0; ht < 2; ++ht) {
+                bf16x8 aw = *(const bf16x8*)&fc1w[(size_t)(ch*128 + wv*32 + ht*16 + l15)*128 + ks*32 + quad*8];
+#pragma unroll
+                for (int tt = 0; tt < 4; ++tt)
+                    ha[ht][tt] = MFMA16(aw, bx[tt], ha[ht][tt]);
+            }
+        }
+#pragma unroll
+        for (int ht = 0; ht < 2; ++ht) {
+            const float4 bb4 = *(const float4*)&fc1bf[ch*128 + wv*32 + ht*16 + quad*4];
+            const int hb = wv*32 + ht*16 + quad*4;
+#pragma unroll
+            for (int tt = 0; tt < 4; ++tt) {
+                float hv[4];
 #pragma unroll
                 for (int r = 0; r < 4; ++r) {
-                    float v = ha[mt][nt][r] + bb;
-                    v = v / (1.0f + __expf(-v));
-                    hs[(mt*16 + quad*4 + r)*136 + hl] = (bf16)v;
-                }
+                    float v = ha[ht][tt][r] + ((const float*)&bb4)[r];
+                    hv[r] = v / (1.0f + __expf(-v));
+                }
+                pack4(hv[0], hv[1], hv[2], hv[3], &hs[(tt*16 + l15)*136 + hb]);
+            }
         }
         __syncthreads();
 #pragma unroll
         for (int ks = 0; ks < 4; ++ks) {
-            bf16x8 ah[4];
-#pragma unroll
-            for (int mt = 0; mt < 4; ++mt)
-                ah[mt] = *(const bf16x8*)&hs[(mt*16 + l15)*136 + ks*32 + quad*8];
-#pragma unroll
-            for (int nt = 0; nt < 2; ++nt) {
-                const int oc = wv*32 + nt*16 + l15;
-                bf16x8 bw = *(const bf16x8*)&fc2w[(size_t)oc*512 + ch*128 + ks*32 + quad*8];
-#pragma unroll
-                for (int mt = 0; mt < 4; ++mt)
-                    ya[mt][nt] = MFMA16(ah[mt], bw, ya[mt][nt]);
-            }
-        }
-    }
-    __syncthreads();
-
-    {
-        float pb[2], wn[2], bn[2];
-#pragma unroll
-        for (int nt = 0; nt < 2; ++nt) {
-            const int oc = wv*32 + nt*16 + l15;
-            pb[nt] = fc2bf[oc]; wn[nt] = n2wf[oc]; bn[nt] = n2bf[oc];
-        }
-#pragma unroll
-        for (int mt = 0; mt < 4; ++mt)
-#pragma unroll
-            for (int r = 0; r < 4; ++r) {
-                ya[mt][0][r] += pb[0];
-                ya[mt][1][r] += pb[1];
-                float sv = ya[mt][0][r] + ya[mt][1][r];
-                sv += __shfl_xor(sv, 1); sv += __shfl_xor(sv, 2);
-                sv += __shfl_xor(sv, 4); sv += __shfl_xor(sv, 8);
-                if (l15 == 0) psum[wv*64 + mt*16 + quad*4 + r] = sv;
-            }
-        __syncthreads();
-        float mu[4][4];
-#pragma unroll
-        for (int mt = 0; mt < 4; ++mt)
-#pragma unroll
-            for (int r = 0; r < 4; ++r) {
-                const int i = mt*16 + quad*4 + r;
-                mu[mt][r] = (psum[i] + psum[64+i] + psum[128+i] + psum[192+i]) * (1.0f/128.0f);
-                const float d0 = ya[mt][0][r] - mu[mt][r];
-                const float d1 = ya[mt][1][r] - mu[mt][r];
-                float sv = d0*d0 + d1*d1;
-                sv += __shfl_xor(sv, 1); sv += __shfl_xor(sv, 2);
-                sv += __shfl_xor(sv, 4); sv += __shfl_xor(sv, 8);
-                if (l15 == 0) pvar[wv*64 + i] = sv;
-            }
+            bf16x8 bh[4];
+#pragma unroll
+            for (int tt = 0; tt < 4; ++tt)
+                bh[tt] = *(const bf16x8*)&hs[(tt*16 + l15)*136 + ks*32 + quad*8];
+#pragma unroll
+            for (int ct = 0; ct < 2; ++ct) {
+                bf16x8 aw = *(const bf16x8*)&fc2w[(size_t)(wv*32 + ct*16 + l15)*512 + ch*128 + ks*32 + quad*8];
+#pragma unroll
+                for (int tt = 0; tt < 4; ++tt)
+                    ya[ct][tt] = MFMA16(aw, bh[tt], ya[ct][tt]);
+            }
+        }
+    }
+    __syncthreads();
+
+    {
+        float4 pb4[2], wn4[2], bn4[2];
+#pragma unroll
+        for (int ct = 0; ct < 2; ++ct) {
+            const int ob = wv*32 + ct*16 + quad*4;
+            pb4[ct] = *(const float4*)&fc2bf[ob];
+            wn4[ct] = *(const float4*)&n2wf[ob];
+            bn4[ct] = *(const float4*)&n2bf[ob];
+        }
+#pragma unroll
+        for (int tt = 0; tt < 4; ++tt) {
+            float sv = 0.f;
+#pragma unroll
+            for (int ct = 0; ct < 2; ++ct)
+#pragma unroll
+                for (int r = 0; r < 4; ++r) {
+                    ya[ct][tt][r] += ((const float*)&pb4[ct])[r];
+                    sv += ya[ct][tt][r];
+                }
+            sv += __shfl_xor(sv, 16);
+            sv += __shfl_xor(sv, 32);
+            if (quad == 0) psum[wv*64 + tt*16 + l15] = sv;
+        }
+        __syncthreads();
+        float mu[4];
+#pragma unroll
+        for (int tt = 0; tt < 4; ++tt) {
+            const int tok = tt*16 + l15;
+            mu[tt] = (psum[tok] + psum[64+tok] + psum[128+tok] + psum[192+tok]) * (1.0f/128.0f);
+            float sv = 0.f;
+#pragma unroll
+            for (int ct = 0; ct < 2; ++ct)
+#pragma unroll
+                for (int r = 0; r < 4; ++r) {
+                    const float d = ya[ct][tt][r] - mu[tt];
+                    sv += d*d;
+                }
+            sv += __shfl_xor(sv, 16);
+            sv += __shfl_xor(sv, 32);
+            if (quad == 0) pvar[wv*64 + tok] = sv;
+        }
         __syncthreads();
         bf16* x2s = hs;
 #pragma unroll
-        for (int mt = 0; mt < 4; ++mt)
-#pragma unroll
-            for (int r = 0; r < 4; ++r) {
-                const int i = mt*16 + quad*4 + r;
-                const float var = (pvar[i] + pvar[64+i] + pvar[128+i] + pvar[192+i]) * (1.0f/128.0f);
-                const float rstd = rsqrtf(var + 1e-5f);
-#pragma unroll
-                for (int nt = 0; nt < 2; ++nt) {
-                    const int oc = wv*32 + nt*16 + l15;
-                    const float yv = (ya[mt][nt][r] - mu[mt][r]) * rstd * wn[nt] + bn[nt];
-                    const float x2v = bf2f(x1s[i*136 + oc]) + yv;
-                    x2s[i*136 + oc] = (bf16)x2v;
-                }
-            }
+        for (int tt = 0; tt < 4; ++tt) {
+            const int tok = tt*16 + l15;
+            const float var = (pvar[tok] + pvar[64+tok] + pvar[128+tok] + pvar[192+tok]) * (1.0f/128.0f);
+            const float rstd = rsqrtf(var + 1e-5f);
+#pragma unroll
+            for (int ct = 0; ct < 2; ++ct) {
+                const int ob = wv*32 + ct*16 + quad*4;
+                bf16x4 xr = *(const bf16x4*)&x1s[tok*136 + ob];
+                float xv[4];
+#pragma unroll
+                for (int r = 0; r < 4; ++r)
+                    xv[r] = bf2f(xr[r]) + (ya[ct][tt][r] - mu[tt]) * rstd * ((const float*)&wn4[ct])[r]
+                            + ((const float*)&bn4[ct])[r];
+                pack4(xv[0], xv[1], xv[2], xv[3], &x2s[tok*136 + ob]);
+            }
+        }
     }
     __syncthreads();
 
@@ -597,7 +620,7 @@
             const int rr = idx >> 7;
             const int hf = (wh*8 + rr + 4) & 127;
             const size_t rowb = ((size_t)(b*128 + c))*16384 + (size_t)hf*128;
-            if constexpr (DT == 0) {
+            if (!isf) {
                 const unsigned short* xu = (const unsigned short*)x2s;
                 uint2 u0, u1;
                 u0.x = (unsigned)xu[(rr*8+0)*136 + c] | ((unsigned)xu[(rr*8+1)*136 + c] << 16);
@@ -650,20 +673,11 @@
     float* scales  = (float*)(ws + OFF_SCALES);
     int*   flag    = (int*)(ws + OFF_FLAG);
 
-    k_precompute<<<dim3(1), dim3(256), 0, stream>>>(cpb_w1, cpb_b1, cpb_w2, lscale, qkv_w,
-                                                    biasAll, scales, flag);
-    k_convert<<<dim3(96), dim3(256), 0, stream>>>(qkv_w, proj_w, fc1w, fc2w,
-                                                  q_bias, v_bias, proj_b, n1w, n1b,
-                                                  fc1b, fc2b, n2w, n2b, flag, ws);
-    k_fused<0><<<dim3(4096), dim3(256), 0, stream>>>(x,
-        (const bf16*)(ws + OFF_QKVW), (const float*)(ws + OFF_QKVB),
-        (const bf16*)(ws + OFF_PROJW), (const float*)(ws + OFF_PROJB),
-        (const float*)(ws + OFF_N1W), (const float*)(ws + OFF_N1B),
-        (const bf16*)(ws + OFF_FC1W), (const float*)(ws + OFF_FC1B),
-        (const bf16*)(ws + OFF_FC2W), (const float*)(ws + OFF_FC2B),
-        (const float*)(ws + OFF_N2W), (const float*)(ws + OFF_N2B),
-        biasAll, scales, flag, d_out);
-    k_fused<1><<<dim3(4096), dim3(256), 0, stream>>>(x,
+    k_init<<<dim3(97), dim3(256), 0, stream>>>(cpb_w1, cpb_b1, cpb_w2, lscale,
+                                               qkv_w, proj_w, fc1w, fc2w,
+                                               q_bias, v_bias, proj_b, n1w, n1b,
+                                               fc1b, fc2b, n2w, n2b, ws);
+    k_fused<<<dim3(4096), dim3(256), 0, stream>>>(x,
         (const bf16*)(ws + OFF_QKVW), (const float*)(ws + OFF_QKVB),
         (const bf16*)(ws + OFF_PROJW), (const float*)(ws + OFF_PROJB),
         (const float*)(ws + OFF_N1W), (const float*)(ws + OFF_N1B),
```

Measured after the change: 588.2 us. -16.1%, faster.
